# Kernel optimization log

Measured on AMD Instinct MI355X. Metric: run time of the kernel, lower is better.

## Reference

```python
import jax, jax.numpy as jnp
import numpy as np

B, T, H = 128, 64, 128  # batch == decoder_num_hidden == encoder_num_hidden (forced by the module's math)


def setup_inputs() -> dict:
    key = jax.random.key(0)
    ks = jax.random.split(key, 14)
    f = lambda k, s: jax.random.normal(k, s, dtype=jnp.float32)
    W_SCALE = 0.05  # keep tanh/sigmoid/softmax away from saturation
    return {
        "X_encoded": f(ks[0], (B, T, H)),
        "X_tilde": f(ks[1], (B, T, H)),
        "W1": f(ks[2], (H, 3 * H)) * W_SCALE,   # attn_layer Linear(2*dec+enc -> enc)
        "b1": f(ks[3], (H,)) * W_SCALE,
        "W2": f(ks[4], (1, H)) * W_SCALE,        # attn_layer Linear(enc -> 1)
        "b2": f(ks[5], (1,)) * W_SCALE,
        "Wfc": f(ks[6], (1, 2 * H)) * W_SCALE,   # fc Linear(2*dec -> 1)
        "bfc": f(ks[7], (1,)) * W_SCALE,
        "Wih": f(ks[8], (4 * H, 1)) * W_SCALE,   # LSTM weight_ih, input_size=1
        "bih": f(ks[9], (4 * H,)) * W_SCALE,
        "Whh": f(ks[10], (4 * H, H)) * W_SCALE,  # LSTM weight_hh
        "bhh": f(ks[11], (4 * H,)) * W_SCALE,
        "Wfin": f(ks[12], (1, 2 * H)) * W_SCALE, # fc_final Linear(dec+enc -> 1)
        "bfin": f(ks[13], (1,)) * W_SCALE,
    }


def reference(X_encoded, X_tilde, W1, b1, W2, b2, Wfc, bfc, Wih, bih, Whh, bhh, Wfin, bfin):
    Bv, Tv, E = X_encoded.shape
    Hd = Whh.shape[1]

    def step(carry, xt):
        h, cc, _ = carry  # h: hidden d_n [B,Hd], cc: cell c_n [B,Hd]
        # x = cat(d_n broadcast over T, c_n broadcast over T, X_encoded) -> [B,T,2Hd+E]
        x = jnp.concatenate([
            jnp.broadcast_to(h[:, None, :], (Bv, Tv, Hd)),
            jnp.broadcast_to(cc[:, None, :], (Bv, Tv, Hd)),
            X_encoded], axis=2)
        a = jnp.tanh(x @ W1.T + b1) @ W2.T + b2      # [B,T,1]
        beta = jax.nn.softmax(a[..., 0], axis=1)       # [B,T]
        context = jnp.einsum('bt,bte->be', beta, X_encoded)  # [B,E]
        # cat along dim 0 then transpose: feature axis of fc is the doubled batch axis
        y = jnp.concatenate([context, xt], axis=0).T @ Wfc.T + bfc  # [E,1]
        # LSTM cell (PyTorch gate order i,f,g,o); LSTM batch == E == B
        gates = y @ Wih.T + bih + h @ Whh.T + bhh     # [E,4Hd]
        i, fg, g, o = jnp.split(gates, 4, axis=1)
        cc2 = jax.nn.sigmoid(fg) * cc + jax.nn.sigmoid(i) * jnp.tanh(g)
        h2 = jax.nn.sigmoid(o) * jnp.tanh(cc2)
        return (h2, cc2, context), None

    init = (jnp.zeros((Bv, Hd), X_encoded.dtype),
            jnp.zeros((Bv, Hd), X_encoded.dtype),
            jnp.zeros((Bv, E), X_encoded.dtype))
    (h, cc, context), _ = jax.lax.scan(step, init, jnp.swapaxes(X_tilde, 0, 1))
    return jnp.concatenate([h, context], axis=1) @ Wfin.T + bfin  # [B,1]
```

## Files before the change

kernel.cpp:

```cpp
#include <hip/hip_runtime.h>

#define TT 64
#define HD 128
#define BB 128
#define G  64
#define RPB 2
#define NT 512

__device__ __forceinline__ float fast_rcp(float x){ return __builtin_amdgcn_rcpf(x); }
__device__ __forceinline__ float fast_tanh(float x){
    float e = __expf(2.f*x);
    return 1.f - 2.f*__builtin_amdgcn_rcpf(e+1.f);
}
__device__ __forceinline__ float fast_sigmoid(float x){
    return __builtin_amdgcn_rcpf(1.f + __expf(-x));
}


__global__ void k_prep(const float* __restrict__ W1, const float* __restrict__ Whh,
                       float* __restrict__ W1T, float* __restrict__ WhhT,
                       unsigned int* __restrict__ flags){
    int idx = blockIdx.x*blockDim.x + threadIdx.x;
    int stride = gridDim.x*blockDim.x;
    for (int i=idx; i<384*HD; i+=stride){ int m=i>>7, k=i&127; W1T[i] = W1[k*384+m]; }
    for (int i=idx; i<512*HD; i+=stride){ int k=i>>9, j=i&511; WhhT[i] = Whh[j*HD+k]; }
    for (int i=idx; i<TT*G;   i+=stride) flags[i] = 0u;
}

__global__ void k_pre(const float* __restrict__ Xe, const float* __restrict__ W1T,
                      const float* __restrict__ b1, float* __restrict__ preE){
    __shared__ float sX[2][HD];
    const int tid = threadIdx.x;
    const int rr = tid>>7, k = tid&127;
    const int row0 = blockIdx.x*32;
    const float* wp = W1T + 256*HD + k;
    const float bk = b1[k];
    for (int it=0; it<16; ++it){
        int row = row0 + it*2 + rr;
        sX[rr][k] = Xe[row*HD + k];
        __syncthreads();
        float a0=0.f, a1=0.f;
        #pragma unroll 8
        for (int j=0;j<HD;j+=2){
            a0 += sX[rr][j]   * wp[(j)*HD];
            a1 += sX[rr][j+1] * wp[(j+1)*HD];
        }
        preE[row*HD + k] = a0 + a1 + bk;
        __syncthreads();
    }
}

__global__ void k_xtw(const float* __restrict__ Xt, const float* __restrict__ Wfc,
                      const float* __restrict__ bfc, float* __restrict__ xtw){
    const int t = blockIdx.x;
    const int e = threadIdx.x;
    float a0=0.f, a1=0.f;
    for (int b=0;b<BB;b+=2){
        a0 += Xt[(b*TT     + t)*HD + e] * Wfc[128+b];
        a1 += Xt[((b+1)*TT + t)*HD + e] * Wfc[129+b];
    }
    xtw[t*HD + e] = a0 + a1 + bfc[0];
}

__global__ __launch_bounds__(NT, 1) void k_loop(
    const float* __restrict__ Xe, const float* __restrict__ preE,
    const float* __restrict__ W1T, const float* __restrict__ WhhT,
    const float* __restrict__ xtw,
    const float* __restrict__ W2, const float* __restrict__ b2,
    const float* __restrict__ Wfc,
    const float* __restrict__ Wih, const float* __restrict__ bih,
    const float* __restrict__ bhh,
    const float* __restrict__ Wfin, const float* __restrict__ bfin,
    float* __restrict__ ctxbuf, unsigned int* __restrict__ flags,
    float* __restrict__ out)
{
    __shared__ float sh[RPB][HD], scc[RPB][HD], shW1[RPB][HD];
    __shared__ float sa[RPB][TT], sbeta[RPB][TT];
    __shared__ float sctx[RPB][HD];
    __shared__ float gh[RPB][512];
    __shared__ float red[NT];
    __shared__ float sW2[HD], sWfc[HD], sWih[512], sbihh[512], sWfin[2*HD];
    __shared__ float sy[RPB];
    __shared__ float sb2;

    const int tid = threadIdx.x;
    const int g   = blockIdx.x;
    const int b0  = g*RPB;

    for (int i=tid;i<HD;i+=NT){ sW2[i]=W2[i]; sWfc[i]=Wfc[i]; }
    for (int i=tid;i<512;i+=NT){ sWih[i]=Wih[i]; sbihh[i]=bih[i]+bhh[i]; }
    for (int i=tid;i<2*HD;i+=NT){ sWfin[i]=Wfin[i]; }
    for (int i=tid;i<RPB*HD;i+=NT){ (&sh[0][0])[i]=0.f; (&scc[0][0])[i]=0.f; }
    if (tid==0) sb2 = b2[0];
    __syncthreads();

    for (int t=0;t<TT;t++){
        {
            const int mh = tid>>8;
            const int rr = (tid>>7)&1;
            const int k  = tid&127;
            const float* xv = mh ? scc[rr] : sh[rr];
            const float* wp = W1T + (mh*HD)*HD + k;
            float a0=0.f, a1=0.f;
            #pragma unroll 8
            for (int m=0;m<HD;m+=2){
                a0 += xv[m]   * wp[(m)*HD];
                a1 += xv[m+1] * wp[(m+1)*HD];
            }
            red[tid] = a0+a1;
        }
        __syncthreads();
        if (tid<256){
            const int rr = tid>>7, k = tid&127;
            shW1[rr][k] = red[tid] + red[tid+256];
        }
        __syncthreads();

        {
            const int rr = tid>>8;
            const int rest = tid&255;
            const int tp = rest>>2;
            const int kp = rest&3;
            const int k0 = kp*32;
            const float4* pe4 = (const float4*)(preE + ((b0+rr)*TT + tp)*HD + k0);
            float acc=0.f;
            #pragma unroll
            for (int q=0;q<8;q++){
                float4 v = pe4[q];
                int k = k0 + q*4;
                acc += sW2[k+0]*fast_tanh(v.x + shW1[rr][k+0]);
                acc += sW2[k+1]*fast_tanh(v.y + shW1[rr][k+1]);
                acc += sW2[k+2]*fast_tanh(v.z + shW1[rr][k+2]);
                acc += sW2[k+3]*fast_tanh(v.w + shW1[rr][k+3]);
            }
            acc += __shfl_xor(acc,1);
            acc += __shfl_xor(acc,2);
            if (kp==0) sa[rr][tp] = acc + sb2;
        }
        __syncthreads();

        if (tid<2*TT){
            const int rr = tid>>6, l = tid&63;
            float v = sa[rr][l];
            float mx = v;
            #pragma unroll
            for (int d=32;d;d>>=1) mx = fmaxf(mx, __shfl_xor(mx,d));
            float e = __expf(v-mx);
            float s = e;
            #pragma unroll
            for (int d=32;d;d>>=1) s += __shfl_xor(s,d);
            sbeta[rr][l] = e * fast_rcp(s);
        }
        __syncthreads();

        {
            const int rr = tid>>8;
            const int rest = tid&255;
            const int tp = rest>>7;
            const int e = rest&127;
            const float* xr = Xe + ((b0+rr)*TT + tp*32)*HD + e;
            float acc=0.f;
            #pragma unroll 8
            for (int q=0;q<32;q++) acc += sbeta[rr][tp*32+q] * xr[q*HD];
            red[tid]=acc;
        }
        __syncthreads();
        if (tid<256){
            const int rr = tid>>7, e = tid&127;
            float c = red[rr*256 + e] + red[rr*256 + 128 + e];
            sctx[rr][e] = c;
            __hip_atomic_store(&ctxbuf[((t&1)*BB + b0+rr)*HD + e], c,
                               __ATOMIC_RELAXED, __HIP_MEMORY_SCOPE_AGENT);
        }
        __syncthreads();
        if (tid==0)
            __hip_atomic_store(&flags[t*G + g], 1u, __ATOMIC_RELAXED, __HIP_MEMORY_SCOPE_AGENT);

        {
            const float* wp = WhhT + tid;
            float a0=0.f, a1=0.f;
            #pragma unroll 4
            for (int k=0;k<HD;k++){
                float w = wp[k*512];
                a0 += w*sh[0][k];
                a1 += w*sh[1][k];
            }
            gh[0][tid]=a0; gh[1][tid]=a1;
        }

        if (tid<G){
            const unsigned int* fp = flags + t*G;
            while (!__all(__hip_atomic_load(&fp[tid], __ATOMIC_RELAXED, __HIP_MEMORY_SCOPE_AGENT) != 0u))
                __builtin_amdgcn_s_sleep(1);
        }
        __syncthreads();

        if (tid<256){
            const int rr = tid>>7, bp = tid&127;
            float c = __hip_atomic_load(&ctxbuf[((t&1)*BB + bp)*HD + (b0+rr)],
                                        __ATOMIC_RELAXED, __HIP_MEMORY_SCOPE_AGENT);
            float p = c * sWfc[bp];
            #pragma unroll
            for (int d=32;d;d>>=1) p += __shfl_xor(p,d);
            if ((tid&63)==0) red[tid>>6]=p;
        }
        __syncthreads();
        if (tid<RPB) sy[tid] = red[2*tid]+red[2*tid+1] + xtw[t*HD + b0+tid];
        __syncthreads();

        if (tid<256){
            const int rr = tid>>7, u = tid&127;
            const float yv = sy[rr];
            float gi = gh[rr][u      ] + yv*sWih[u      ] + sbihh[u      ];
            float gf = gh[rr][128+u  ] + yv*sWih[128+u  ] + sbihh[128+u  ];
            float gg = gh[rr][256+u  ] + yv*sWih[256+u  ] + sbihh[256+u  ];
            float go = gh[rr][384+u  ] + yv*sWih[384+u  ] + sbihh[384+u  ];
            float c2 = fast_sigmoid(gf)*scc[rr][u] + fast_sigmoid(gi)*fast_tanh(gg);
            float h2 = fast_sigmoid(go)*fast_tanh(c2);
            scc[rr][u]=c2; sh[rr][u]=h2;
        }
        __syncthreads();
    }

    if (tid<256){
        const int rr = tid>>7, u = tid&127;
        float p = sh[rr][u]*sWfin[u] + sctx[rr][u]*sWfin[HD+u];
        #pragma unroll
        for (int d=32;d;d>>=1) p += __shfl_xor(p,d);
        if ((tid&63)==0) red[tid>>6]=p;
    }
    __syncthreads();
    if (tid<RPB) out[b0+tid] = red[2*tid]+red[2*tid+1] + bfin[0];
}

extern "C" void kernel_launch(void* const* d_in, const int* in_sizes, int n_in,
                              void* d_out, int out_size, void* d_ws, size_t ws_size,
                              hipStream_t stream){
    const float* Xe  = (const float*)d_in[0];
    const float* Xt  = (const float*)d_in[1];
    const float* W1  = (const float*)d_in[2];
    const float* b1  = (const float*)d_in[3];
    const float* W2  = (const float*)d_in[4];
    const float* b2  = (const float*)d_in[5];
    const float* Wfc = (const float*)d_in[6];
    const float* bfc = (const float*)d_in[7];
    const float* Wih = (const float*)d_in[8];
    const float* bih = (const float*)d_in[9];
    const float* Whh = (const float*)d_in[10];
    const float* bhh = (const float*)d_in[11];
    const float* Wfin= (const float*)d_in[12];
    const float* bfin= (const float*)d_in[13];

    float* ws     = (float*)d_ws;
    float* preE   = ws;
    float* W1T    = preE   + (size_t)BB*TT*HD;
    float* WhhT   = W1T    + 384*HD;
    float* xtw    = WhhT   + 512*HD;
    float* ctxbuf = xtw    + TT*HD;
    unsigned int* flags = (unsigned int*)(ctxbuf + 2*BB*HD);
    float* outp   = (float*)d_out;

    hipLaunchKernelGGL(k_prep, dim3(128), dim3(256), 0, stream, W1, Whh, W1T, WhhT, flags);
    hipLaunchKernelGGL(k_pre,  dim3(256), dim3(256), 0, stream, Xe, W1T, b1, preE);
    hipLaunchKernelGGL(k_xtw,  dim3(64),  dim3(128), 0, stream, Xt, Wfc, bfc, xtw);
    hipLaunchKernelGGL(k_loop, dim3(G),   dim3(NT),  0, stream,
        Xe, preE, W1T, WhhT, xtw, W2, b2, Wfc, Wih, bih, bhh, Wfin, bfin,
        ctxbuf, flags, outp);
}
```

Baseline: 777.7 us.

## Rewrite recurrent kernel: one batch row per block, register-resident weights, atomic-add cross-block reduction

The loop kernel now uses 128 blocks, each handling one batch row instead of two. Each block keeps its slices of W1 and Whh in registers and its preE and X_encoded tiles in LDS (64 KB dynamic shared memory), so the weight transposes and repeated global reads disappear. The all-to-all context exchange through a ctxbuf with per-block flags becomes an atomicAdd into y followed by a single counter barrier per timestep. The prep kernels are also reworked to read W1 directly. The cost is heavy register pressure (about 192 floats per thread) and a grid-wide spin barrier that now needs all 128 blocks co-resident.

```diff
diff --git a/kernel.cpp b/kernel.cpp
--- a/kernel.cpp
+++ b/kernel.cpp
@@ -1,11 +1,10 @@
 #include <hip/hip_runtime.h>
 
-#define TT 64
-#define HD 128
-#define BB 128
-#define G  64
-#define RPB 2
-#define NT 512
+#define TT   64
+#define HD   128
+#define BB   128
+#define NBLK 128
+#define NT   512
 
 __device__ __forceinline__ float fast_rcp(float x){ return __builtin_amdgcn_rcpf(x); }
 __device__ __forceinline__ float fast_tanh(float x){
@@ -17,220 +16,210 @@
 }
 
 
-__global__ void k_prep(const float* __restrict__ W1, const float* __restrict__ Whh,
-                       float* __restrict__ W1T, float* __restrict__ WhhT,
-                       unsigned int* __restrict__ flags){
-    int idx = blockIdx.x*blockDim.x + threadIdx.x;
-    int stride = gridDim.x*blockDim.x;
-    for (int i=idx; i<384*HD; i+=stride){ int m=i>>7, k=i&127; W1T[i] = W1[k*384+m]; }
-    for (int i=idx; i<512*HD; i+=stride){ int k=i>>9, j=i&511; WhhT[i] = Whh[j*HD+k]; }
-    for (int i=idx; i<TT*G;   i+=stride) flags[i] = 0u;
-}
-
-__global__ void k_pre(const float* __restrict__ Xe, const float* __restrict__ W1T,
-                      const float* __restrict__ b1, float* __restrict__ preE){
-    __shared__ float sX[2][HD];
+__global__ void k_prep(unsigned int* __restrict__ cnt){
+    if (threadIdx.x < TT) cnt[threadIdx.x] = 0u;
+}
+
+__global__ __launch_bounds__(256) void k_pre(const float* __restrict__ Xe,
+    const float* __restrict__ W1, const float* __restrict__ b1,
+    float* __restrict__ preE){
+    __shared__ float2 sx2[16*HD];
+    __shared__ float  red[512];
     const int tid = threadIdx.x;
-    const int rr = tid>>7, k = tid&127;
-    const int row0 = blockIdx.x*32;
-    const float* wp = W1T + 256*HD + k;
-    const float bk = b1[k];
-    for (int it=0; it<16; ++it){
-        int row = row0 + it*2 + rr;
-        sX[rr][k] = Xe[row*HD + k];
-        __syncthreads();
+    const int k = tid & 127, q = tid >> 7;
+    const int r0 = blockIdx.x * 32;
+    float wv[64];
+    { const float4* wp = (const float4*)(W1 + (size_t)k*384 + 256 + q*64);
+      #pragma unroll
+      for (int c=0;c<16;c++){ float4 v=wp[c]; wv[4*c]=v.x; wv[4*c+1]=v.y; wv[4*c+2]=v.z; wv[4*c+3]=v.w; } }
+    const float b1k = b1[k];
+    float* sxf = (float*)sx2;
+    for (int i=tid; i<32*HD; i+=256){
+        int row = i>>7, m = i&127;
+        sxf[((row>>1)*HD + m)*2 + (row&1)] = Xe[(size_t)(r0+row)*HD + m];
+    }
+    __syncthreads();
+    for (int p=0;p<16;p++){
+        const float2* xp = sx2 + p*HD + q*64;
         float a0=0.f, a1=0.f;
-        #pragma unroll 8
-        for (int j=0;j<HD;j+=2){
-            a0 += sX[rr][j]   * wp[(j)*HD];
-            a1 += sX[rr][j+1] * wp[(j+1)*HD];
-        }
-        preE[row*HD + k] = a0 + a1 + bk;
-        __syncthreads();
-    }
-}
-
-__global__ void k_xtw(const float* __restrict__ Xt, const float* __restrict__ Wfc,
-                      const float* __restrict__ bfc, float* __restrict__ xtw){
-    const int t = blockIdx.x;
-    const int e = threadIdx.x;
-    float a0=0.f, a1=0.f;
-    for (int b=0;b<BB;b+=2){
-        a0 += Xt[(b*TT     + t)*HD + e] * Wfc[128+b];
-        a1 += Xt[((b+1)*TT + t)*HD + e] * Wfc[129+b];
-    }
-    xtw[t*HD + e] = a0 + a1 + bfc[0];
-}
-
-__global__ __launch_bounds__(NT, 1) void k_loop(
+        #pragma unroll
+        for (int i=0;i<64;i++){ float2 xv = xp[i]; a0 += xv.x*wv[i]; a1 += xv.y*wv[i]; }
+        red[tid] = a0; red[256+tid] = a1;
+        __syncthreads();
+        if (tid<128){
+            float s0 = red[tid]     + red[128+tid];
+            float s1 = red[256+tid] + red[384+tid];
+            preE[(size_t)(r0+2*p  )*HD + tid] = s0 + b1k;
+            preE[(size_t)(r0+2*p+1)*HD + tid] = s1 + b1k;
+        }
+        __syncthreads();
+    }
+}
+
+__global__ __launch_bounds__(128) void k_y(const float* __restrict__ Xt,
+    const float* __restrict__ Wfc, const float* __restrict__ bfc,
+    float* __restrict__ y){
+    const int t = blockIdx.x, e = threadIdx.x;
+    float acc = bfc[0];
+    #pragma unroll 8
+    for (int b=0;b<BB;b++)
+        acc += Xt[((size_t)b*TT + t)*HD + e] * Wfc[BB+b];
+    y[t*HD + e] = acc;
+}
+
+__global__ __launch_bounds__(NT,1) void k_loop(
     const float* __restrict__ Xe, const float* __restrict__ preE,
-    const float* __restrict__ W1T, const float* __restrict__ WhhT,
-    const float* __restrict__ xtw,
+    const float* __restrict__ W1, const float* __restrict__ Whh,
     const float* __restrict__ W2, const float* __restrict__ b2,
     const float* __restrict__ Wfc,
     const float* __restrict__ Wih, const float* __restrict__ bih,
     const float* __restrict__ bhh,
     const float* __restrict__ Wfin, const float* __restrict__ bfin,
-    float* __restrict__ ctxbuf, unsigned int* __restrict__ flags,
+    float* __restrict__ y, unsigned int* __restrict__ cnt,
     float* __restrict__ out)
 {
-    __shared__ float sh[RPB][HD], scc[RPB][HD], shW1[RPB][HD];
-    __shared__ float sa[RPB][TT], sbeta[RPB][TT];
-    __shared__ float sctx[RPB][HD];
-    __shared__ float gh[RPB][512];
+    extern __shared__ __align__(16) float dyn[];
+    float* preEl = dyn;
+    float* Xel   = dyn + TT*HD;
+    __shared__ float4 shv[64];
+    __shared__ __align__(16) float shW1[HD];
+    __shared__ __align__(16) float sW2[HD];
+    __shared__ float sa[TT], sbeta[TT];
+    __shared__ float sctx[HD];
     __shared__ float red[NT];
-    __shared__ float sW2[HD], sWfc[HD], sWih[512], sbihh[512], sWfin[2*HD];
-    __shared__ float sy[RPB];
-    __shared__ float sb2;
+    __shared__ float sWfin[2*HD], sWih[NT], sbihh[NT];
+    __shared__ float sy[1];
+    float* sh = (float*)shv;
 
     const int tid = threadIdx.x;
     const int g   = blockIdx.x;
-    const int b0  = g*RPB;
-
-    for (int i=tid;i<HD;i+=NT){ sW2[i]=W2[i]; sWfc[i]=Wfc[i]; }
-    for (int i=tid;i<512;i+=NT){ sWih[i]=Wih[i]; sbihh[i]=bih[i]+bhh[i]; }
-    for (int i=tid;i<2*HD;i+=NT){ sWfin[i]=Wfin[i]; }
-    for (int i=tid;i<RPB*HD;i+=NT){ (&sh[0][0])[i]=0.f; (&scc[0][0])[i]=0.f; }
-    if (tid==0) sb2 = b2[0];
+    const int k = tid & 127, q = tid >> 7;
+
+    { const float4* s1 = (const float4*)(preE + (size_t)g*TT*HD);
+      const float4* s2 = (const float4*)(Xe   + (size_t)g*TT*HD);
+      float4* d1 = (float4*)preEl; float4* d2 = (float4*)Xel;
+      for (int i=tid; i<TT*HD/4; i+=NT){ d1[i]=s1[i]; d2[i]=s2[i]; } }
+    sWih[tid]  = Wih[tid];
+    sbihh[tid] = bih[tid] + bhh[tid];
+    if (tid < HD)   sW2[tid]  = W2[tid];
+    if (tid < 2*HD) sWfin[tid]= Wfin[tid];
+    if (tid < 2*HD) sh[tid]   = 0.f;
+    const float b2v  = b2[0];
+    const float wfcg = Wfc[g];
+
+    float w1r[64];
+    { const float4* wp = (const float4*)(W1 + (size_t)k*384 + q*64);
+      #pragma unroll
+      for (int c=0;c<16;c++){ float4 v=wp[c]; w1r[4*c]=v.x; w1r[4*c+1]=v.y; w1r[4*c+2]=v.z; w1r[4*c+3]=v.w; } }
+    float whr[128];
+    { const float4* wp = (const float4*)(Whh + (size_t)tid*HD);
+      #pragma unroll
+      for (int c=0;c<32;c++){ float4 v=wp[c]; whr[4*c]=v.x; whr[4*c+1]=v.y; whr[4*c+2]=v.z; whr[4*c+3]=v.w; } }
     __syncthreads();
 
     for (int t=0;t<TT;t++){
         {
-            const int mh = tid>>8;
-            const int rr = (tid>>7)&1;
-            const int k  = tid&127;
-            const float* xv = mh ? scc[rr] : sh[rr];
-            const float* wp = W1T + (mh*HD)*HD + k;
-            float a0=0.f, a1=0.f;
-            #pragma unroll 8
-            for (int m=0;m<HD;m+=2){
-                a0 += xv[m]   * wp[(m)*HD];
-                a1 += xv[m+1] * wp[(m+1)*HD];
-            }
-            red[tid] = a0+a1;
-        }
-        __syncthreads();
-        if (tid<256){
-            const int rr = tid>>7, k = tid&127;
-            shW1[rr][k] = red[tid] + red[tid+256];
-        }
-        __syncthreads();
-
-        {
-            const int rr = tid>>8;
-            const int rest = tid&255;
-            const int tp = rest>>2;
-            const int kp = rest&3;
-            const int k0 = kp*32;
-            const float4* pe4 = (const float4*)(preE + ((b0+rr)*TT + tp)*HD + k0);
+            const float4* xp = (const float4*)(sh + q*64);
             float acc=0.f;
             #pragma unroll
-            for (int q=0;q<8;q++){
-                float4 v = pe4[q];
-                int k = k0 + q*4;
-                acc += sW2[k+0]*fast_tanh(v.x + shW1[rr][k+0]);
-                acc += sW2[k+1]*fast_tanh(v.y + shW1[rr][k+1]);
-                acc += sW2[k+2]*fast_tanh(v.z + shW1[rr][k+2]);
-                acc += sW2[k+3]*fast_tanh(v.w + shW1[rr][k+3]);
-            }
-            acc += __shfl_xor(acc,1);
-            acc += __shfl_xor(acc,2);
-            if (kp==0) sa[rr][tp] = acc + sb2;
-        }
-        __syncthreads();
-
-        if (tid<2*TT){
-            const int rr = tid>>6, l = tid&63;
-            float v = sa[rr][l];
-            float mx = v;
-            #pragma unroll
-            for (int d=32;d;d>>=1) mx = fmaxf(mx, __shfl_xor(mx,d));
-            float e = __expf(v-mx);
-            float s = e;
-            #pragma unroll
-            for (int d=32;d;d>>=1) s += __shfl_xor(s,d);
-            sbeta[rr][l] = e * fast_rcp(s);
-        }
-        __syncthreads();
-
-        {
-            const int rr = tid>>8;
-            const int rest = tid&255;
-            const int tp = rest>>7;
-            const int e = rest&127;
-            const float* xr = Xe + ((b0+rr)*TT + tp*32)*HD + e;
+            for (int c=0;c<16;c++){
+                float4 xv = xp[c];
+                acc += xv.x*w1r[4*c] + xv.y*w1r[4*c+1] + xv.z*w1r[4*c+2] + xv.w*w1r[4*c+3];
+            }
+            red[tid]=acc;
+        }
+        __syncthreads();
+        if (tid<HD) shW1[tid] = red[tid]+red[HD+tid]+red[2*HD+tid]+red[3*HD+tid];
+        __syncthreads();
+
+        {
+            const int tp = tid>>3, kp = tid&7, k0 = kp*16;
+            const float4* pe = (const float4*)(preEl + tp*HD + k0);
+            const float4* hw = (const float4*)(shW1 + k0);
+            const float4* w2 = (const float4*)(sW2 + k0);
             float acc=0.f;
-            #pragma unroll 8
-            for (int q=0;q<32;q++) acc += sbeta[rr][tp*32+q] * xr[q*HD];
+            #pragma unroll
+            for (int c=0;c<4;c++){
+                float4 p4=pe[c], h4=hw[c], w4=w2[c];
+                acc += w4.x*fast_tanh(p4.x+h4.x);
+                acc += w4.y*fast_tanh(p4.y+h4.y);
+                acc += w4.z*fast_tanh(p4.z+h4.z);
+                acc += w4.w*fast_tanh(p4.w+h4.w);
+            }
+            acc += __shfl_xor(acc,1); acc += __shfl_xor(acc,2); acc += __shfl_xor(acc,4);
+            if (kp==0) sa[tp] = acc + b2v;
+        }
+        __syncthreads();
+
+        if (tid<TT){
+            float v = sa[tid];
+            float mx=v;
+            #pragma unroll
+            for (int d=32;d;d>>=1) mx=fmaxf(mx,__shfl_xor(mx,d));
+            float e=__expf(v-mx);
+            float s=e;
+            #pragma unroll
+            for (int d=32;d;d>>=1) s+=__shfl_xor(s,d);
+            sbeta[tid]=e*fast_rcp(s);
+        }
+        __syncthreads();
+
+        {
+            const int e=tid&127, tq=tid>>7;
+            float acc=0.f;
+            #pragma unroll
+            for (int c=0;c<16;c++){
+                int tp = tq*16+c;
+                acc += sbeta[tp]*Xel[tp*HD+e];
+            }
             red[tid]=acc;
         }
         __syncthreads();
-        if (tid<256){
-            const int rr = tid>>7, e = tid&127;
-            float c = red[rr*256 + e] + red[rr*256 + 128 + e];
-            sctx[rr][e] = c;
-            __hip_atomic_store(&ctxbuf[((t&1)*BB + b0+rr)*HD + e], c,
-                               __ATOMIC_RELAXED, __HIP_MEMORY_SCOPE_AGENT);
-        }
-        __syncthreads();
-        if (tid==0)
-            __hip_atomic_store(&flags[t*G + g], 1u, __ATOMIC_RELAXED, __HIP_MEMORY_SCOPE_AGENT);
-
-        {
-            const float* wp = WhhT + tid;
-            float a0=0.f, a1=0.f;
-            #pragma unroll 4
-            for (int k=0;k<HD;k++){
-                float w = wp[k*512];
-                a0 += w*sh[0][k];
-                a1 += w*sh[1][k];
-            }
-            gh[0][tid]=a0; gh[1][tid]=a1;
-        }
-
-        if (tid<G){
-            const unsigned int* fp = flags + t*G;
-            while (!__all(__hip_atomic_load(&fp[tid], __ATOMIC_RELAXED, __HIP_MEMORY_SCOPE_AGENT) != 0u))
+        if (tid<HD){
+            float cv = red[tid]+red[HD+tid]+red[2*HD+tid]+red[3*HD+tid];
+            sctx[tid]=cv;
+            unsafeAtomicAdd(&y[t*HD + tid], cv*wfcg);
+        }
+
+        float gj=0.f;
+        {
+            const float4* hp = (const float4*)sh;
+            #pragma unroll
+            for (int c=0;c<32;c++){
+                float4 hv=hp[c];
+                gj += hv.x*whr[4*c]+hv.y*whr[4*c+1]+hv.z*whr[4*c+2]+hv.w*whr[4*c+3];
+            }
+        }
+        asm volatile("s_waitcnt vmcnt(0)" ::: "memory");
+        __syncthreads();
+        if (tid==0){
+            __hip_atomic_fetch_add(&cnt[t], 1u, __ATOMIC_RELAXED, __HIP_MEMORY_SCOPE_AGENT);
+            while (__hip_atomic_load(&cnt[t], __ATOMIC_RELAXED, __HIP_MEMORY_SCOPE_AGENT) != (unsigned)NBLK)
                 __builtin_amdgcn_s_sleep(1);
-        }
-        __syncthreads();
-
-        if (tid<256){
-            const int rr = tid>>7, bp = tid&127;
-            float c = __hip_atomic_load(&ctxbuf[((t&1)*BB + bp)*HD + (b0+rr)],
-                                        __ATOMIC_RELAXED, __HIP_MEMORY_SCOPE_AGENT);
-            float p = c * sWfc[bp];
-            #pragma unroll
-            for (int d=32;d;d>>=1) p += __shfl_xor(p,d);
-            if ((tid&63)==0) red[tid>>6]=p;
-        }
-        __syncthreads();
-        if (tid<RPB) sy[tid] = red[2*tid]+red[2*tid+1] + xtw[t*HD + b0+tid];
-        __syncthreads();
-
-        if (tid<256){
-            const int rr = tid>>7, u = tid&127;
-            const float yv = sy[rr];
-            float gi = gh[rr][u      ] + yv*sWih[u      ] + sbihh[u      ];
-            float gf = gh[rr][128+u  ] + yv*sWih[128+u  ] + sbihh[128+u  ];
-            float gg = gh[rr][256+u  ] + yv*sWih[256+u  ] + sbihh[256+u  ];
-            float go = gh[rr][384+u  ] + yv*sWih[384+u  ] + sbihh[384+u  ];
-            float c2 = fast_sigmoid(gf)*scc[rr][u] + fast_sigmoid(gi)*fast_tanh(gg);
+            sy[0] = __hip_atomic_load(&y[t*HD + g], __ATOMIC_RELAXED, __HIP_MEMORY_SCOPE_AGENT);
+        }
+        __syncthreads();
+
+        red[tid] = gj + sy[0]*sWih[tid] + sbihh[tid];
+        __syncthreads();
+        if (tid<HD){
+            float gi=red[tid], gf=red[HD+tid], gg=red[2*HD+tid], go=red[3*HD+tid];
+            float cold = sh[HD+tid];
+            float c2 = fast_sigmoid(gf)*cold + fast_sigmoid(gi)*fast_tanh(gg);
             float h2 = fast_sigmoid(go)*fast_tanh(c2);
-            scc[rr][u]=c2; sh[rr][u]=h2;
-        }
-        __syncthreads();
-    }
-
-    if (tid<256){
-        const int rr = tid>>7, u = tid&127;
-        float p = sh[rr][u]*sWfin[u] + sctx[rr][u]*sWfin[HD+u];
+            sh[tid]=h2; sh[HD+tid]=c2;
+        }
+        __syncthreads();
+    }
+
+    if (tid<HD){
+        float p = sh[tid]*sWfin[tid] + sctx[tid]*sWfin[HD+tid];
         #pragma unroll
         for (int d=32;d;d>>=1) p += __shfl_xor(p,d);
         if ((tid&63)==0) red[tid>>6]=p;
     }
     __syncthreads();
-    if (tid<RPB) out[b0+tid] = red[2*tid]+red[2*tid+1] + bfin[0];
+    if (tid==0) out[g] = red[0]+red[1]+bfin[0];
 }
 
 extern "C" void kernel_launch(void* const* d_in, const int* in_sizes, int n_in,
@@ -251,19 +240,16 @@
     const float* Wfin= (const float*)d_in[12];
     const float* bfin= (const float*)d_in[13];
 
-    float* ws     = (float*)d_ws;
-    float* preE   = ws;
-    float* W1T    = preE   + (size_t)BB*TT*HD;
-    float* WhhT   = W1T    + 384*HD;
-    float* xtw    = WhhT   + 512*HD;
-    float* ctxbuf = xtw    + TT*HD;
-    unsigned int* flags = (unsigned int*)(ctxbuf + 2*BB*HD);
-    float* outp   = (float*)d_out;
-
-    hipLaunchKernelGGL(k_prep, dim3(128), dim3(256), 0, stream, W1, Whh, W1T, WhhT, flags);
-    hipLaunchKernelGGL(k_pre,  dim3(256), dim3(256), 0, stream, Xe, W1T, b1, preE);
-    hipLaunchKernelGGL(k_xtw,  dim3(64),  dim3(128), 0, stream, Xt, Wfc, bfc, xtw);
-    hipLaunchKernelGGL(k_loop, dim3(G),   dim3(NT),  0, stream,
-        Xe, preE, W1T, WhhT, xtw, W2, b2, Wfc, Wih, bih, bhh, Wfin, bfin,
-        ctxbuf, flags, outp);
-}
+    float* ws   = (float*)d_ws;
+    float* preE = ws;
+    float* y    = preE + (size_t)BB*TT*HD;
+    unsigned int* cnt = (unsigned int*)(y + TT*HD);
+    float* outp = (float*)d_out;
+
+    hipLaunchKernelGGL(k_prep, dim3(1),    dim3(64),  0, stream, cnt);
+    hipLaunchKernelGGL(k_pre,  dim3(256),  dim3(256), 0, stream, Xe, W1, b1, preE);
+    hipLaunchKernelGGL(k_y,    dim3(TT),   dim3(128), 0, stream, Xt, Wfc, bfc, y);
+    hipLaunchKernelGGL(k_loop, dim3(NBLK), dim3(NT),  2*TT*HD*sizeof(float), stream,
+        Xe, preE, W1, Whh, W2, b2, Wfc, Wih, bih, bhh, Wfin, bfin,
+        y, cnt, outp);
+}
```

Measured after the change: 1.040 ms. 1.34x slower.
